# Kernel tuning notes

Measured on AMD Instinct MI355X. Metric: run time of the kernel, lower is better.

## Reference

```python
import jax, jax.numpy as jnp
import numpy as np


def setup_inputs() -> dict:
    key = jax.random.key(0)
    k0, k1, k2 = jax.random.split(key, 3)
    B, N, C, H = 4, 4096, 384, 192  # H = encoder_channel // 2
    point = jax.random.normal(k0, (B, N, 3), dtype=jnp.float32)
    W1 = jax.random.normal(k1, (6, H), dtype=jnp.float32) * (1.0 / np.sqrt(6.0))
    b1 = jnp.zeros((H,), dtype=jnp.float32)
    W2 = jax.random.normal(k2, (H, C), dtype=jnp.float32) * (1.0 / np.sqrt(H))
    b2 = jnp.zeros((C,), dtype=jnp.float32)
    return {"point": point, "W1": W1, "b1": b1, "W2": W2, "b2": b2, "k": 16}


def reference(point, W1, b1, W2, b2, k):
    # point: [B, N, 3]
    # pairwise squared distances [B, N, N]
    diff = point[:, :, None, :] - point[:, None, :, :]
    dist = jnp.sum(diff * diff, axis=-1)
    # torch: distance.argsort()[:, :, :k]  (includes self as nearest)
    idx = jnp.argsort(dist, axis=-1)[:, :, :k]          # [B, N, k]
    # gather neighbor coordinates per batch: [B, N, k, 3]
    neigh = jax.vmap(lambda p, i: p[i])(point, idx)
    rel = neigh - point[:, :, None, :]                   # relative coords
    ctr = jnp.broadcast_to(point[:, :, None, :], rel.shape)
    f = jnp.concatenate([rel, ctr], axis=-1)             # [B, N, k, 6]
    # Mlp: fc1 -> swish -> fc2 (dropout p=0)
    h = f @ W1 + b1
    h = h * jax.nn.sigmoid(h)
    h = h @ W2 + b2                                      # [B, N, k, C]
    return jnp.max(h, axis=-2)                           # [B, N, C]
```

## Files before the change

kernel.cpp:

```cpp
#include <hip/hip_runtime.h>

#define NPTS 4096
#define NBATCH 4
#define HDIM 192
#define CDIM 384

typedef _Float16 f16x8 __attribute__((ext_vector_type(8)));
typedef float f32x4 __attribute__((ext_vector_type(4)));

__global__ __launch_bounds__(256) void prep_w2(const float* __restrict__ W2,
                                               _Float16* __restrict__ W2F) {
  const int j = blockIdx.x * 256 + threadIdx.x;
  if (j < 9216) {
    const int lane = j & 63, r = lane & 15, kg = lane >> 4;
    const int kt = (j >> 6) % 6, ct = j / 384;
    const int c = ct * 16 + r, h0 = kt * 32 + kg * 8;
    f16x8 v;
#pragma unroll
    for (int e = 0; e < 8; ++e) v[e] = (_Float16)W2[(size_t)(h0 + e) * CDIM + c];
    *(f16x8*)(W2F + (size_t)j * 8) = v;
  }
}

#define SCAP 30
#define FINF 3.4e38f

#define PRUNE()                                                                      \
  do {                                                                               \
    int mc = cnt;                                                                    \
    _Pragma("unroll")                                                                \
    for (int s = 32; s; s >>= 1) { int o = __shfl_xor(mc, s); mc = mc > o ? mc : o; }\
    mc = __builtin_amdgcn_readfirstlane(mc);                                         \
    for (int e = 0; e < mc; ++e) {                                                   \
      const int j = sstk[sbase + e] & 4095;                                          \
      const float dx = qx - spx[j];                                                  \
      const float dy = qy - spy[j];                                                  \
      const float dz = qz - spz[j];                                                  \
      const float d = __fadd_rn(__fadd_rn(__fmul_rn(dx, dx), __fmul_rn(dy, dy)),     \
                                __fmul_rn(dz, dz));                                  \
      const float v = (e < cnt && d < dl[15]) ? d : FINF;                            \
      bool cc[16];                                                                   \
      _Pragma("unroll")                                                              \
      for (int i = 0; i < 16; ++i) cc[i] = v < dl[i];                                \
      _Pragma("unroll")                                                              \
      for (int i = 15; i >= 1; --i) {                                                \
        dl[i] = cc[i] ? (cc[i - 1] ? dl[i - 1] : v) : dl[i];                         \
        il[i] = cc[i] ? (cc[i - 1] ? il[i - 1] : j) : il[i];                         \
      }                                                                              \
      dl[0] = cc[0] ? v : dl[0];                                                     \
      il[0] = cc[0] ? j : il[0];                                                     \
    }                                                                                \
    cnt = 0;                                                                         \
    thr = dl[15];                                                                    \
    atomicMin(&sThrU[ql], __float_as_uint(dl[15]));                                  \
  } while (0)

__global__ __launch_bounds__(512) void knn_kernel(const float* __restrict__ pts,
                                                  int* __restrict__ idx_out) {
  __shared__ float smem[12352];
  __shared__ float sstk_f[7680];
  __shared__ unsigned sThrU[32];
  unsigned short* sstk = (unsigned short*)sstk_f;

  float* spx = smem;
  float* spy = smem + 4096;
  float* spz = smem + 8192;

  const int t  = threadIdx.x;
  const int b  = blockIdx.x >> 7;
  const int qb = (blockIdx.x & 127) << 5;
  const float* P = pts + (size_t)b * NPTS * 3;

  for (int i = t; i < NPTS; i += 512) {
    spx[i] = P[3 * i + 0];
    spy[i] = P[3 * i + 1];
    spz[i] = P[3 * i + 2];
  }
  if (t < 32) sThrU[t] = __float_as_uint(FINF);
  __syncthreads();

  const int ql    = t & 31;
  const int q     = qb + ql;
  const int cid   = (t >> 5) & 15;
  const int cbase = cid << 8;
  const float qx = spx[q], qy = spy[q], qz = spz[q];

  float dl[16];
  int   il[16];
#pragma unroll
  for (int i = 0; i < 16; ++i) { dl[i] = FINF; il[i] = 0; }
  float thr = FINF;
  int   cnt = 0;
  const int sbase = t * SCAP;

  for (int jt = 0; jt < 256; jt += 8) {
    {
      const unsigned tb = ((volatile unsigned*)sThrU)[ql];
      thr = fminf(dl[15], __uint_as_float(tb));
    }
    const int jb = cbase + jt;
    const f32x4 x0 = *(const f32x4*)(spx + jb);
    const f32x4 x1 = *(const f32x4*)(spx + jb + 4);
    const f32x4 y0 = *(const f32x4*)(spy + jb);
    const f32x4 y1 = *(const f32x4*)(spy + jb + 4);
    const f32x4 z0 = *(const f32x4*)(spz + jb);
    const f32x4 z1 = *(const f32x4*)(spz + jb + 4);
#pragma unroll
    for (int u = 0; u < 8; ++u) {
      const float px = (u < 4) ? x0[u & 3] : x1[u & 3];
      const float py = (u < 4) ? y0[u & 3] : y1[u & 3];
      const float pz = (u < 4) ? z0[u & 3] : z1[u & 3];
      const float dx = qx - px;
      const float dy = qy - py;
      const float dz = qz - pz;
      const float d = __fadd_rn(__fadd_rn(__fmul_rn(dx, dx), __fmul_rn(dy, dy)),
                                __fmul_rn(dz, dz));
      if (d <= thr) { sstk[sbase + cnt] = (unsigned short)(jb + u); ++cnt; }
    }
    if (__any(cnt >= SCAP - 8)) PRUNE();
  }
  PRUNE();

  __syncthreads();

  float*          md = smem;
  unsigned short* mi = (unsigned short*)(smem + 8224);
  const int lbase = ql * 257 + cid * 16;
#pragma unroll
  for (int i = 0; i < 16; ++i) {
    md[lbase + i] = dl[i];
    mi[lbase + i] = (unsigned short)il[i];
  }
  __syncthreads();

  float*          od = sstk_f;
  unsigned short* oi = (unsigned short*)(sstk_f + 2080);
  if (t < 128) {
    const int mq = t >> 2, g = t & 3;
    const int base = mq * 257 + g * 64;
    int p0 = 0, p1 = 0, p2 = 0, p3 = 0;
    const int ob = mq * 65 + g * 16;
    for (int r = 0; r < 16; ++r) {
      const float d0 = md[base + p0];
      const float d1 = md[base + 16 + p1];
      const float d2 = md[base + 32 + p2];
      const float d3 = md[base + 48 + p3];
      int bw = 0; float bd = d0;
      if (d1 < bd) { bd = d1; bw = 1; }
      if (d2 < bd) { bd = d2; bw = 2; }
      if (d3 < bd) { bd = d3; bw = 3; }
      const unsigned short bi = (bw == 0) ? mi[base + p0]
                              : (bw == 1) ? mi[base + 16 + p1]
                              : (bw == 2) ? mi[base + 32 + p2]
                                          : mi[base + 48 + p3];
      od[ob + r] = bd;
      oi[ob + r] = bi;
      p0 += (bw == 0); p1 += (bw == 1); p2 += (bw == 2); p3 += (bw == 3);
    }
  }
  __syncthreads();

  if (t < 32) {
    const int base = t * 65;
    int p0 = 0, p1 = 0, p2 = 0, p3 = 0;
    int* op = idx_out + (((size_t)b * NPTS + qb + t) << 4);
    for (int r = 0; r < 16; ++r) {
      const float d0 = od[base + p0];
      const float d1 = od[base + 16 + p1];
      const float d2 = od[base + 32 + p2];
      const float d3 = od[base + 48 + p3];
      int bw = 0; float bd = d0;
      if (d1 < bd) { bd = d1; bw = 1; }
      if (d2 < bd) { bd = d2; bw = 2; }
      if (d3 < bd) { bd = d3; bw = 3; }
      const unsigned short bi = (bw == 0) ? oi[base + p0]
                              : (bw == 1) ? oi[base + 16 + p1]
                              : (bw == 2) ? oi[base + 32 + p2]
                                          : oi[base + 48 + p3];
      op[r] = (int)bi;
      p0 += (bw == 0); p1 += (bw == 1); p2 += (bw == 2); p3 += (bw == 3);
    }
  }
}

__global__ __launch_bounds__(512) void mlp_kernel(const float* __restrict__ pts,
                                                  const int* __restrict__ idx,
                                                  const float* __restrict__ W1,
                                                  const float* __restrict__ b1,
                                                  const _Float16* __restrict__ W2F,
                                                  const float* __restrict__ b2,
                                                  float* __restrict__ out) {
  __shared__ _Float16 sB[73728];

  const int bid = blockIdx.x;
  const int b   = bid >> 7;
  const int t   = threadIdx.x;
  const int wv  = t >> 6;
  const int q0  = ((bid & 127) << 5) + (wv << 2);
  const float* P = pts + (size_t)b * NPTS * 3;
  const int l   = t & 63;
  const int r   = l & 15;
  const int kg  = l >> 4;

#pragma unroll
  for (int i = 0; i < 18; ++i) {
    const int j = i * 512 + t;
    *(f16x8*)(sB + (size_t)j * 8) = *(const f16x8*)(W2F + (size_t)j * 8);
  }

  float f[4][6];
#pragma unroll
  for (int qi = 0; qi < 4; ++qi) {
    const int qq = q0 + qi;
    const int nb = idx[(((size_t)b * NPTS + qq) << 4) + r];
    const float ax = P[qq * 3 + 0], ay = P[qq * 3 + 1], az = P[qq * 3 + 2];
    f[qi][0] = P[nb * 3 + 0] - ax;
    f[qi][1] = P[nb * 3 + 1] - ay;
    f[qi][2] = P[nb * 3 + 2] - az;
    f[qi][3] = ax; f[qi][4] = ay; f[qi][5] = az;
  }

  f16x8 af[4][6];
#pragma unroll
  for (int kt = 0; kt < 6; ++kt) {
    const int h0 = kt * 32 + kg * 8;
    const f32x4 bb0 = *(const f32x4*)(b1 + h0);
    const f32x4 bb1 = *(const f32x4*)(b1 + h0 + 4);
    f32x4 w0[6], w1[6];
#pragma unroll
    for (int in = 0; in < 6; ++in) {
      w0[in] = *(const f32x4*)(W1 + in * HDIM + h0);
      w1[in] = *(const f32x4*)(W1 + in * HDIM + h0 + 4);
    }
#pragma unroll
    for (int qi = 0; qi < 4; ++qi) {
      f32x4 a0 = bb0, a1 = bb1;
#pragma unroll
      for (int in = 0; in < 6; ++in) {
        a0 += f[qi][in] * w0[in];
        a1 += f[qi][in] * w1[in];
      }
      f16x8 v;
#pragma unroll
      for (int j = 0; j < 4; ++j) {
        v[j]     = (_Float16)(a0[j] * __builtin_amdgcn_rcpf(1.0f + __expf(-a0[j])));
        v[j + 4] = (_Float16)(a1[j] * __builtin_amdgcn_rcpf(1.0f + __expf(-a1[j])));
      }
      af[qi][kt] = v;
    }
  }
  __syncthreads();

  const size_t orow = (size_t)b * NPTS + q0;
  const _Float16* bp = sB + (size_t)l * 8;

  for (int ct = 0; ct < 24; ++ct) {
    const int c = ct * 16 + r;
    f16x8 bfr[6];
#pragma unroll
    for (int kt = 0; kt < 6; ++kt)
      bfr[kt] = *(const f16x8*)(bp + (size_t)(ct * 6 + kt) * 512);

    f32x4 acc[4];
#pragma unroll
    for (int qi = 0; qi < 4; ++qi) acc[qi] = f32x4{0.f, 0.f, 0.f, 0.f};
#pragma unroll
    for (int kt = 0; kt < 6; ++kt)
#pragma unroll
      for (int qi = 0; qi < 4; ++qi)
        acc[qi] = __builtin_amdgcn_mfma_f32_16x16x32_f16(af[qi][kt], bfr[kt], acc[qi], 0, 0, 0);

    const float bb = b2[c];
#pragma unroll
    for (int qi = 0; qi < 4; ++qi) {
      float m = fmaxf(fmaxf(acc[qi][0], acc[qi][1]), fmaxf(acc[qi][2], acc[qi][3]));
      m = fmaxf(m, __shfl_xor(m, 16));
      m = fmaxf(m, __shfl_xor(m, 32));
      if (l < 16)
        out[(orow + qi) * CDIM + c] = m + bb;
    }
  }
}

extern "C" void kernel_launch(void* const* d_in, const int* in_sizes, int n_in,
                              void* d_out, int out_size, void* d_ws, size_t ws_size,
                              hipStream_t stream) {
  const float* point = (const float*)d_in[0];
  const float* W1    = (const float*)d_in[1];
  const float* b1    = (const float*)d_in[2];
  const float* W2    = (const float*)d_in[3];
  const float* b2    = (const float*)d_in[4];

  int*      idx_ws = (int*)d_ws;
  _Float16* W2F    = (_Float16*)((char*)d_ws + (1 << 20));

  prep_w2<<<36, 256, 0, stream>>>(W2, W2F);
  knn_kernel<<<512, 512, 0, stream>>>(point, idx_ws);
  mlp_kernel<<<512, 512, 0, stream>>>(point, idx_ws, W1, b1, W2F, b2, (float*)d_out);
}
```

Before: 149.0 us.

## Sort points by x and prune kNN search slabs by coordinate gap

```diff
diff --git a/kernel.cpp b/kernel.cpp
--- a/kernel.cpp
+++ b/kernel.cpp
@@ -4,6 +4,7 @@
 #define NBATCH 4
 #define HDIM 192
 #define CDIM 384
+#define FINF 3.4e38f
 
 typedef _Float16 f16x8 __attribute__((ext_vector_type(8)));
 typedef float f32x4 __attribute__((ext_vector_type(4)));
@@ -22,162 +23,207 @@
   }
 }
 
-#define SCAP 30
-#define FINF 3.4e38f
-
-#define PRUNE()                                                                      \
-  do {                                                                               \
-    int mc = cnt;                                                                    \
-    _Pragma("unroll")                                                                \
-    for (int s = 32; s; s >>= 1) { int o = __shfl_xor(mc, s); mc = mc > o ? mc : o; }\
-    mc = __builtin_amdgcn_readfirstlane(mc);                                         \
-    for (int e = 0; e < mc; ++e) {                                                   \
-      const int j = sstk[sbase + e] & 4095;                                          \
-      const float dx = qx - spx[j];                                                  \
-      const float dy = qy - spy[j];                                                  \
-      const float dz = qz - spz[j];                                                  \
-      const float d = __fadd_rn(__fadd_rn(__fmul_rn(dx, dx), __fmul_rn(dy, dy)),     \
-                                __fmul_rn(dz, dz));                                  \
-      const float v = (e < cnt && d < dl[15]) ? d : FINF;                            \
-      bool cc[16];                                                                   \
-      _Pragma("unroll")                                                              \
-      for (int i = 0; i < 16; ++i) cc[i] = v < dl[i];                                \
-      _Pragma("unroll")                                                              \
-      for (int i = 15; i >= 1; --i) {                                                \
-        dl[i] = cc[i] ? (cc[i - 1] ? dl[i - 1] : v) : dl[i];                         \
-        il[i] = cc[i] ? (cc[i - 1] ? il[i - 1] : j) : il[i];                         \
-      }                                                                              \
-      dl[0] = cc[0] ? v : dl[0];                                                     \
-      il[0] = cc[0] ? j : il[0];                                                     \
-    }                                                                                \
-    cnt = 0;                                                                         \
-    thr = dl[15];                                                                    \
-    atomicMin(&sThrU[ql], __float_as_uint(dl[15]));                                  \
+__global__ __launch_bounds__(1024) void sort_kernel(const float* __restrict__ pts,
+                                                    float4* __restrict__ sp4) {
+  __shared__ float kx[4096];
+  __shared__ int   ki[4096];
+  const int b = blockIdx.x;
+  const float* P = pts + (size_t)b * NPTS * 3;
+  const int t = threadIdx.x;
+  for (int i = t; i < 4096; i += 1024) { kx[i] = P[3 * i]; ki[i] = i; }
+  __syncthreads();
+  for (int k = 2; k <= 4096; k <<= 1) {
+    for (int jj = k >> 1; jj > 0; jj >>= 1) {
+      for (int m = t; m < 2048; m += 1024) {
+        const int i = ((m & ~(jj - 1)) << 1) | (m & (jj - 1));
+        const int p = i | jj;
+        const bool up = (i & k) == 0;
+        const float xi = kx[i], xp = kx[p];
+        const int   ii = ki[i], ip = ki[p];
+        const bool gt = (xi > xp) || (xi == xp && ii > ip);
+        if (gt == up) { kx[i] = xp; kx[p] = xi; ki[i] = ip; ki[p] = ii; }
+      }
+      __syncthreads();
+    }
+  }
+  for (int i = t; i < 4096; i += 1024) {
+    const int j = ki[i];
+    sp4[(size_t)b * 4096 + i] =
+        make_float4(P[3 * j], P[3 * j + 1], P[3 * j + 2], __uint_as_float((unsigned)j));
+  }
+}
+
+#define KSCAP 32
+
+#define PRUNE2()                                                                      \
+  do {                                                                                \
+    int mc = cnt;                                                                     \
+    _Pragma("unroll")                                                                 \
+    for (int s_ = 32; s_; s_ >>= 1) { int o_ = __shfl_xor(mc, s_); mc = mc > o_ ? mc : o_; } \
+    mc = __builtin_amdgcn_readfirstlane(mc);                                          \
+    for (int e = 0; e < mc; ++e) {                                                    \
+      const bool act = (e < cnt);                                                     \
+      const float    dd = act ? dstk[e * 512 + t] : FINF;                             \
+      const unsigned jj = act ? (unsigned)jstk[e * 512 + t] : 0xFFFFFFFFu;            \
+      bool cc[16];                                                                    \
+      _Pragma("unroll")                                                               \
+      for (int i = 0; i < 16; ++i)                                                    \
+        cc[i] = (dd < dl[i]) || (dd == dl[i] && jj < il[i]);                          \
+      _Pragma("unroll")                                                               \
+      for (int i = 15; i >= 1; --i) {                                                 \
+        dl[i] = cc[i] ? (cc[i - 1] ? dl[i - 1] : dd) : dl[i];                         \
+        il[i] = cc[i] ? (cc[i - 1] ? il[i - 1] : jj) : il[i];                         \
+      }                                                                               \
+      dl[0] = cc[0] ? dd : dl[0];                                                     \
+      il[0] = cc[0] ? jj : il[0];                                                     \
+    }                                                                                 \
+    cnt = 0;                                                                          \
+    thr = dl[15];                                                                     \
+    atomicMin(&sThrU[l], __float_as_uint(dl[15]));                                    \
   } while (0)
 
-__global__ __launch_bounds__(512) void knn_kernel(const float* __restrict__ pts,
+#define PROC_SLAB(S)                                                                  \
+  do {                                                                                \
+    slab[wv][l] = SP[(S) * 64 + l];               \
+    for (int c0 = 0; c0 < 64; c0 += 16) {                                             \
+      const float te = fminf(thr, __uint_as_float(((volatile unsigned*)sThrU)[l]));   \
+      _Pragma("unroll")                                                               \
+      for (int c = c0; c < c0 + 16; ++c) {                                            \
+        const float4 pc = slab[wv][c];                                                \
+        const float dx = qx - pc.x;                                                   \
+        const float dy = qy - pc.y;                                                   \
+        const float dz = qz - pc.z;                                                   \
+                  \
+        const float d = __fadd_rn(__fadd_rn(__fmul_rn(dx, dx), __fmul_rn(dy, dy)),    \
+                                  __fmul_rn(dz, dz));                                 \
+        if (d <= te) {                                                                \
+          dstk[cnt * 512 + t] = d;                                                    \
+          jstk[cnt * 512 + t] = (unsigned short)__float_as_uint(pc.w);                \
+          ++cnt;                                                                      \
+        }                                                                             \
+      }                                                                               \
+      if (__any(cnt >= KSCAP - 16)) PRUNE2();                                         \
+    }                                                                                 \
+  } while (0)
+
+__global__ __launch_bounds__(512) void knn_kernel(const float4* __restrict__ sp4,
                                                   int* __restrict__ idx_out) {
-  __shared__ float smem[12352];
-  __shared__ float sstk_f[7680];
-  __shared__ unsigned sThrU[32];
-  unsigned short* sstk = (unsigned short*)sstk_f;
-
-  float* spx = smem;
-  float* spy = smem + 4096;
-  float* spz = smem + 8192;
-
-  const int t  = threadIdx.x;
-  const int b  = blockIdx.x >> 7;
-  const int qb = (blockIdx.x & 127) << 5;
-  const float* P = pts + (size_t)b * NPTS * 3;
-
-  for (int i = t; i < NPTS; i += 512) {
-    spx[i] = P[3 * i + 0];
-    spy[i] = P[3 * i + 1];
-    spz[i] = P[3 * i + 2];
-  }
-  if (t < 32) sThrU[t] = __float_as_uint(FINF);
-  __syncthreads();
-
-  const int ql    = t & 31;
-  const int q     = qb + ql;
-  const int cid   = (t >> 5) & 15;
-  const int cbase = cid << 8;
-  const float qx = spx[q], qy = spy[q], qz = spz[q];
-
-  float dl[16];
-  int   il[16];
-#pragma unroll
-  for (int i = 0; i < 16; ++i) { dl[i] = FINF; il[i] = 0; }
+  __shared__ float          dstk[KSCAP * 512];
+  __shared__ unsigned short jstk[KSCAP * 512];
+  __shared__ unsigned       sThrU[64];
+  __shared__ float4         slab[8][64];
+
+  const int bid = blockIdx.x;
+  const int b = bid >> 6, g = bid & 63;
+  const float4* SP = sp4 + (size_t)b * 4096;
+  const int t = threadIdx.x, wv = t >> 6, l = t & 63;
+
+  if (t < 64) sThrU[t] = __float_as_uint(FINF);
+  __syncthreads();
+
+  const float4 me = SP[g * 64 + l];
+  const float qx = me.x, qy = me.y, qz = me.z;
+  const unsigned origq = __float_as_uint(me.w);
+
+  float    dl[16];
+  unsigned il[16];
+#pragma unroll
+  for (int i = 0; i < 16; ++i) { dl[i] = FINF; il[i] = 0xFFFFFFFFu; }
   float thr = FINF;
   int   cnt = 0;
-  const int sbase = t * SCAP;
-
-  for (int jt = 0; jt < 256; jt += 8) {
-    {
-      const unsigned tb = ((volatile unsigned*)sThrU)[ql];
-      thr = fminf(dl[15], __uint_as_float(tb));
-    }
-    const int jb = cbase + jt;
-    const f32x4 x0 = *(const f32x4*)(spx + jb);
-    const f32x4 x1 = *(const f32x4*)(spx + jb + 4);
-    const f32x4 y0 = *(const f32x4*)(spy + jb);
-    const f32x4 y1 = *(const f32x4*)(spy + jb + 4);
-    const f32x4 z0 = *(const f32x4*)(spz + jb);
-    const f32x4 z1 = *(const f32x4*)(spz + jb + 4);
-#pragma unroll
-    for (int u = 0; u < 8; ++u) {
-      const float px = (u < 4) ? x0[u & 3] : x1[u & 3];
-      const float py = (u < 4) ? y0[u & 3] : y1[u & 3];
-      const float pz = (u < 4) ? z0[u & 3] : z1[u & 3];
-      const float dx = qx - px;
-      const float dy = qy - py;
-      const float dz = qz - pz;
-      const float d = __fadd_rn(__fadd_rn(__fmul_rn(dx, dx), __fmul_rn(dy, dy)),
-                                __fmul_rn(dz, dz));
-      if (d <= thr) { sstk[sbase + cnt] = (unsigned short)(jb + u); ++cnt; }
-    }
-    if (__any(cnt >= SCAP - 8)) PRUNE();
-  }
-  PRUNE();
-
-  __syncthreads();
-
-  float*          md = smem;
-  unsigned short* mi = (unsigned short*)(smem + 8224);
-  const int lbase = ql * 257 + cid * 16;
-#pragma unroll
-  for (int i = 0; i < 16; ++i) {
-    md[lbase + i] = dl[i];
-    mi[lbase + i] = (unsigned short)il[i];
-  }
-  __syncthreads();
-
-  float*          od = sstk_f;
-  unsigned short* oi = (unsigned short*)(sstk_f + 2080);
-  if (t < 128) {
-    const int mq = t >> 2, g = t & 3;
-    const int base = mq * 257 + g * 64;
+
+  int  oHi = wv;
+  int  oLo = (wv == 0) ? 8 : wv;
+  bool hiOpen = (g + oHi) < 64;
+  bool loOpen = (g - oLo) >= 0;
+
+  while (hiOpen || loOpen) {
+    if (hiOpen) {
+      const int s = g + oHi;
+      bool skip = false;
+      if (oHi > 0) {
+        const float bx  = SP[s * 64].x;
+        const float gap = bx - qx;
+        const float te  = fminf(thr, __uint_as_float(((volatile unsigned*)sThrU)[l]));
+        skip = __all(__fmul_rn(gap, gap) > te * 1.0001f + 1e-6f);
+      }
+      if (skip) hiOpen = false;
+      else {
+        PROC_SLAB(s);
+        oHi += 8;
+        if (g + oHi >= 64) hiOpen = false;
+      }
+    }
+    if (loOpen) {
+      const int s = g - oLo;
+      {
+        const float bx  = SP[s * 64 + 63].x;
+        const float gap = qx - bx;
+        const float te  = fminf(thr, __uint_as_float(((volatile unsigned*)sThrU)[l]));
+        if (__all(__fmul_rn(gap, gap) > te * 1.0001f + 1e-6f)) loOpen = false;
+      }
+      if (loOpen) {
+        PROC_SLAB(s);
+        oLo += 8;
+        if (g - oLo < 0) loOpen = false;
+      }
+    }
+  }
+  PRUNE2();
+
+  __syncthreads();
+
+  float*          dm = dstk;
+  unsigned short* jm = jstk;
+  {
+    const int base = l * 129 + wv * 16;
+#pragma unroll
+    for (int i = 0; i < 16; ++i) {
+      dm[base + i] = dl[i];
+      jm[base + i] = (unsigned short)il[i];
+    }
+  }
+  __syncthreads();
+
+  float*          om = dstk + 8320;
+  unsigned short* oj = jstk + 8320;
+  if (t < 256) {
+    const int q = t >> 2, h = t & 3;
+    const int bse = q * 129 + h * 32;
+    int p0 = 0, p1 = 0;
+    const int ob = q * 65 + h * 16;
+    for (int r = 0; r < 16; ++r) {
+      const float d0 = dm[bse + p0];
+      const float d1 = dm[bse + 16 + p1];
+      const unsigned short j0 = jm[bse + p0];
+      const unsigned short j1 = jm[bse + 16 + p1];
+      const bool take1 = (d1 < d0) || (d1 == d0 && j1 < j0);
+      om[ob + r] = take1 ? d1 : d0;
+      oj[ob + r] = take1 ? j1 : j0;
+      p0 += !take1; p1 += take1;
+    }
+  }
+  __syncthreads();
+
+  if (t < 64) {
+    const int bse = t * 65;
     int p0 = 0, p1 = 0, p2 = 0, p3 = 0;
-    const int ob = mq * 65 + g * 16;
+    const unsigned oq = __float_as_uint(SP[g * 64 + t].w);
+    int* op = idx_out + (((size_t)b * NPTS + oq) << 4);
     for (int r = 0; r < 16; ++r) {
-      const float d0 = md[base + p0];
-      const float d1 = md[base + 16 + p1];
-      const float d2 = md[base + 32 + p2];
-      const float d3 = md[base + 48 + p3];
-      int bw = 0; float bd = d0;
-      if (d1 < bd) { bd = d1; bw = 1; }
-      if (d2 < bd) { bd = d2; bw = 2; }
-      if (d3 < bd) { bd = d3; bw = 3; }
-      const unsigned short bi = (bw == 0) ? mi[base + p0]
-                              : (bw == 1) ? mi[base + 16 + p1]
-                              : (bw == 2) ? mi[base + 32 + p2]
-                                          : mi[base + 48 + p3];
-      od[ob + r] = bd;
-      oi[ob + r] = bi;
-      p0 += (bw == 0); p1 += (bw == 1); p2 += (bw == 2); p3 += (bw == 3);
-    }
-  }
-  __syncthreads();
-
-  if (t < 32) {
-    const int base = t * 65;
-    int p0 = 0, p1 = 0, p2 = 0, p3 = 0;
-    int* op = idx_out + (((size_t)b * NPTS + qb + t) << 4);
-    for (int r = 0; r < 16; ++r) {
-      const float d0 = od[base + p0];
-      const float d1 = od[base + 16 + p1];
-      const float d2 = od[base + 32 + p2];
-      const float d3 = od[base + 48 + p3];
-      int bw = 0; float bd = d0;
-      if (d1 < bd) { bd = d1; bw = 1; }
-      if (d2 < bd) { bd = d2; bw = 2; }
-      if (d3 < bd) { bd = d3; bw = 3; }
-      const unsigned short bi = (bw == 0) ? oi[base + p0]
-                              : (bw == 1) ? oi[base + 16 + p1]
-                              : (bw == 2) ? oi[base + 32 + p2]
-                                          : oi[base + 48 + p3];
-      op[r] = (int)bi;
+      const float d0 = om[bse + p0];
+      const float d1 = om[bse + 16 + p1];
+      const float d2 = om[bse + 32 + p2];
+      const float d3 = om[bse + 48 + p3];
+      const unsigned short j0 = oj[bse + p0];
+      const unsigned short j1 = oj[bse + 16 + p1];
+      const unsigned short j2 = oj[bse + 32 + p2];
+      const unsigned short j3 = oj[bse + 48 + p3];
+      float bd = d0; unsigned short bj = j0; int bw = 0;
+      if (d1 < bd || (d1 == bd && j1 < bj)) { bd = d1; bj = j1; bw = 1; }
+      if (d2 < bd || (d2 == bd && j2 < bj)) { bd = d2; bj = j2; bw = 2; }
+      if (d3 < bd || (d3 == bd && j3 < bj)) { bd = d3; bj = j3; bw = 3; }
+      op[r] = (int)bj;
       p0 += (bw == 0); p1 += (bw == 1); p2 += (bw == 2); p3 += (bw == 3);
     }
   }
@@ -292,9 +338,11 @@
   const float* b2    = (const float*)d_in[4];
 
   int*      idx_ws = (int*)d_ws;
-  _Float16* W2F    = (_Float16*)((char*)d_ws + (1 << 20));
+  float4*   sp4    = (float4*)((char*)d_ws + (1 << 20));
+  _Float16* W2F    = (_Float16*)((char*)d_ws + (1 << 20) + (256 << 10));
 
   prep_w2<<<36, 256, 0, stream>>>(W2, W2F);
-  knn_kernel<<<512, 512, 0, stream>>>(point, idx_ws);
+  sort_kernel<<<NBATCH, 1024, 0, stream>>>(point, sp4);
+  knn_kernel<<<256, 512, 0, stream>>>(sp4, idx_ws);
   mlp_kernel<<<512, 512, 0, stream>>>(point, idx_ws, W1, b1, W2F, b2, (float*)d_out);
 }
```

Result: slower. 262.2 us (+76.0%).

## Sort points into x-buckets and prune kNN chunks by bounding gap

Applied to the files above, without the earlier changes.

```diff
diff --git a/kernel.cpp b/kernel.cpp
--- a/kernel.cpp
+++ b/kernel.cpp
@@ -4,6 +4,7 @@
 #define NBATCH 4
 #define HDIM 192
 #define CDIM 384
+#define FINF 3.4e38f
 
 typedef _Float16 f16x8 __attribute__((ext_vector_type(8)));
 typedef float f32x4 __attribute__((ext_vector_type(4)));
@@ -22,100 +23,185 @@
   }
 }
 
-#define SCAP 30
-#define FINF 3.4e38f
+__global__ __launch_bounds__(1024) void bucket_kernel(const float* __restrict__ pts,
+                                                      float4* __restrict__ sp4,
+                                                      float* __restrict__ bnds) {
+  __shared__ float sx[4096];
+  __shared__ float sxs[4096];
+  __shared__ unsigned hist[64];
+  __shared__ float rmn_s[16], rmx_s[16];
+  __shared__ float gmin_s, ginvw_s;
+  const int b = blockIdx.x;
+  const float* P = pts + (size_t)b * NPTS * 3;
+  const int t = threadIdx.x;
+
+  float mn = FINF, mx = -FINF;
+  for (int i = t; i < 4096; i += 1024) {
+    const float x = P[3 * i];
+    sx[i] = x;
+    mn = fminf(mn, x);
+    mx = fmaxf(mx, x);
+  }
+#pragma unroll
+  for (int s = 32; s; s >>= 1) {
+    mn = fminf(mn, __shfl_xor(mn, s));
+    mx = fmaxf(mx, __shfl_xor(mx, s));
+  }
+  if ((t & 63) == 0) { rmn_s[t >> 6] = mn; rmx_s[t >> 6] = mx; }
+  if (t < 64) hist[t] = 0;
+  __syncthreads();
+  if (t == 0) {
+    float gmn = rmn_s[0], gmx = rmx_s[0];
+    for (int i = 1; i < 16; ++i) { gmn = fminf(gmn, rmn_s[i]); gmx = fmaxf(gmx, rmx_s[i]); }
+    gmin_s  = gmn;
+    ginvw_s = (gmx > gmn) ? 64.0f / (gmx - gmn) : 0.0f;
+  }
+  __syncthreads();
+  const float gmn = gmin_s, ginvw = ginvw_s;
+  for (int i = t; i < 4096; i += 1024) {
+    int bn = (int)((sx[i] - gmn) * ginvw);
+    bn = bn < 0 ? 0 : (bn > 63 ? 63 : bn);
+    atomicAdd(&hist[bn], 1u);
+  }
+  __syncthreads();
+  if (t == 0) {
+    unsigned run = 0;
+    for (int i = 0; i < 64; ++i) { const unsigned c = hist[i]; hist[i] = run; run += c; }
+  }
+  __syncthreads();
+  for (int i = t; i < 4096; i += 1024) {
+    const float x = sx[i];
+    int bn = (int)((x - gmn) * ginvw);
+    bn = bn < 0 ? 0 : (bn > 63 ? 63 : bn);
+    const unsigned pos = atomicAdd(&hist[bn], 1u);
+    sp4[(size_t)b * 4096 + pos] =
+        make_float4(x, P[3 * i + 1], P[3 * i + 2], __uint_as_float((unsigned)i));
+    sxs[pos] = x;
+  }
+  __syncthreads();
+  {
+    const int rg = t >> 6, ln = t & 63;
+    float rmn = FINF, rmx = -FINF;
+    for (int k = ln; k < 256; k += 64) {
+      const float v = sxs[rg * 256 + k];
+      rmn = fminf(rmn, v);
+      rmx = fmaxf(rmx, v);
+    }
+#pragma unroll
+    for (int s = 32; s; s >>= 1) {
+      rmn = fminf(rmn, __shfl_xor(rmn, s));
+      rmx = fmaxf(rmx, __shfl_xor(rmx, s));
+    }
+    if (ln == 0) { bnds[b * 32 + rg * 2] = rmn; bnds[b * 32 + rg * 2 + 1] = rmx; }
+  }
+}
+
+#define SCAP 15
 
 #define PRUNE()                                                                      \
   do {                                                                               \
     int mc = cnt;                                                                    \
     _Pragma("unroll")                                                                \
-    for (int s = 32; s; s >>= 1) { int o = __shfl_xor(mc, s); mc = mc > o ? mc : o; }\
+    for (int s_ = 32; s_; s_ >>= 1) { int o_ = __shfl_xor(mc, s_); mc = mc > o_ ? mc : o_; } \
     mc = __builtin_amdgcn_readfirstlane(mc);                                         \
     for (int e = 0; e < mc; ++e) {                                                   \
-      const int j = sstk[sbase + e] & 4095;                                          \
-      const float dx = qx - spx[j];                                                  \
-      const float dy = qy - spy[j];                                                  \
-      const float dz = qz - spz[j];                                                  \
+      const int s = sstk[sbase + e] & 4095;                                          \
+      const float dx = qx - spx[s];                                                  \
+      const float dy = qy - spy[s];                                                  \
+      const float dz = qz - spz[s];                                                  \
       const float d = __fadd_rn(__fadd_rn(__fmul_rn(dx, dx), __fmul_rn(dy, dy)),     \
                                 __fmul_rn(dz, dz));                                  \
-      const float v = (e < cnt && d < dl[15]) ? d : FINF;                            \
+      const bool act = (e < cnt);                                                    \
+      const float    dd = act ? d : FINF;                                            \
+      const unsigned jj = act ? spw[s] : 0xFFFFFFFFu;                                \
       bool cc[16];                                                                   \
       _Pragma("unroll")                                                              \
-      for (int i = 0; i < 16; ++i) cc[i] = v < dl[i];                                \
+      for (int i = 0; i < 16; ++i)                                                   \
+        cc[i] = (dd < dl[i]) || (dd == dl[i] && jj < il[i]);                         \
       _Pragma("unroll")                                                              \
       for (int i = 15; i >= 1; --i) {                                                \
-        dl[i] = cc[i] ? (cc[i - 1] ? dl[i - 1] : v) : dl[i];                         \
-        il[i] = cc[i] ? (cc[i - 1] ? il[i - 1] : j) : il[i];                         \
+        dl[i] = cc[i] ? (cc[i - 1] ? dl[i - 1] : dd) : dl[i];                        \
+        il[i] = cc[i] ? (cc[i - 1] ? il[i - 1] : jj) : il[i];                        \
       }                                                                              \
-      dl[0] = cc[0] ? v : dl[0];                                                     \
-      il[0] = cc[0] ? j : il[0];                                                     \
+      dl[0] = cc[0] ? dd : dl[0];                                                    \
+      il[0] = cc[0] ? jj : il[0];                                                    \
     }                                                                                \
     cnt = 0;                                                                         \
     thr = dl[15];                                                                    \
-    atomicMin(&sThrU[ql], __float_as_uint(dl[15]));                                  \
+    atomicMin(&sThrU[ql], __float_as_uint(thr));                                     \
   } while (0)
 
-__global__ __launch_bounds__(512) void knn_kernel(const float* __restrict__ pts,
+__global__ __launch_bounds__(512) void knn_kernel(const float4* __restrict__ sp4,
+                                                  const float* __restrict__ bnds,
                                                   int* __restrict__ idx_out) {
-  __shared__ float smem[12352];
-  __shared__ float sstk_f[7680];
+  __shared__ float smem[16384];
+  __shared__ unsigned short sstk[7680];
   __shared__ unsigned sThrU[32];
-  unsigned short* sstk = (unsigned short*)sstk_f;
-
-  float* spx = smem;
-  float* spy = smem + 4096;
-  float* spz = smem + 8192;
+
+  float*    spx = smem;
+  float*    spy = smem + 4096;
+  float*    spz = smem + 8192;
+  unsigned* spw = (unsigned*)(smem + 12288);
 
   const int t  = threadIdx.x;
   const int b  = blockIdx.x >> 7;
-  const int qb = (blockIdx.x & 127) << 5;
-  const float* P = pts + (size_t)b * NPTS * 3;
-
-  for (int i = t; i < NPTS; i += 512) {
-    spx[i] = P[3 * i + 0];
-    spy[i] = P[3 * i + 1];
-    spz[i] = P[3 * i + 2];
+  const int g  = blockIdx.x & 127;
+  const float4* SP = sp4 + (size_t)b * 4096;
+
+  for (int i = t; i < 4096; i += 512) {
+    const float4 v = SP[i];
+    spx[i] = v.x; spy[i] = v.y; spz[i] = v.z;
+    spw[i] = __float_as_uint(v.w);
   }
   if (t < 32) sThrU[t] = __float_as_uint(FINF);
   __syncthreads();
 
   const int ql    = t & 31;
-  const int q     = qb + ql;
   const int cid   = (t >> 5) & 15;
   const int cbase = cid << 8;
-  const float qx = spx[q], qy = spy[q], qz = spz[q];
-
-  float dl[16];
-  int   il[16];
-#pragma unroll
-  for (int i = 0; i < 16; ++i) { dl[i] = FINF; il[i] = 0; }
+  const int qpos  = g * 32 + ql;
+  const float qx = spx[qpos], qy = spy[qpos], qz = spz[qpos];
+  const unsigned oq = spw[qpos];
+
+  const float cmin = bnds[b * 32 + cid * 2];
+  const float cmax = bnds[b * 32 + cid * 2 + 1];
+  const float gapc = fmaxf(fmaxf(cmin - qx, qx - cmax), 0.0f);
+  const float g2   = __fmul_rn(gapc, gapc);
+
+  float    dl[16];
+  unsigned il[16];
+#pragma unroll
+  for (int i = 0; i < 16; ++i) { dl[i] = FINF; il[i] = 0xFFFFFFFFu; }
   float thr = FINF;
   int   cnt = 0;
   const int sbase = t * SCAP;
+  bool fin = false;
 
   for (int jt = 0; jt < 256; jt += 8) {
-    {
-      const unsigned tb = ((volatile unsigned*)sThrU)[ql];
-      thr = fminf(dl[15], __uint_as_float(tb));
-    }
-    const int jb = cbase + jt;
-    const f32x4 x0 = *(const f32x4*)(spx + jb);
-    const f32x4 x1 = *(const f32x4*)(spx + jb + 4);
-    const f32x4 y0 = *(const f32x4*)(spy + jb);
-    const f32x4 y1 = *(const f32x4*)(spy + jb + 4);
-    const f32x4 z0 = *(const f32x4*)(spz + jb);
-    const f32x4 z1 = *(const f32x4*)(spz + jb + 4);
-#pragma unroll
-    for (int u = 0; u < 8; ++u) {
-      const float px = (u < 4) ? x0[u & 3] : x1[u & 3];
-      const float py = (u < 4) ? y0[u & 3] : y1[u & 3];
-      const float pz = (u < 4) ? z0[u & 3] : z1[u & 3];
-      const float dx = qx - px;
-      const float dy = qy - py;
-      const float dz = qz - pz;
-      const float d = __fadd_rn(__fadd_rn(__fmul_rn(dx, dx), __fmul_rn(dy, dy)),
-                                __fmul_rn(dz, dz));
-      if (d <= thr) { sstk[sbase + cnt] = (unsigned short)(jb + u); ++cnt; }
+    const unsigned tb = ((volatile unsigned*)sThrU)[ql];
+    const float te = fminf(thr, __uint_as_float(tb));
+    fin = fin || (g2 > te * 1.0001f + 1e-6f);
+    if (__all(fin)) break;
+    if (!fin) {
+      const int jb = cbase + jt;
+      const f32x4 x0 = *(const f32x4*)(spx + jb);
+      const f32x4 x1 = *(const f32x4*)(spx + jb + 4);
+      const f32x4 y0 = *(const f32x4*)(spy + jb);
+      const f32x4 y1 = *(const f32x4*)(spy + jb + 4);
+      const f32x4 z0 = *(const f32x4*)(spz + jb);
+      const f32x4 z1 = *(const f32x4*)(spz + jb + 4);
+#pragma unroll
+      for (int u = 0; u < 8; ++u) {
+        const float px = (u < 4) ? x0[u & 3] : x1[u & 3];
+        const float py = (u < 4) ? y0[u & 3] : y1[u & 3];
+        const float pz = (u < 4) ? z0[u & 3] : z1[u & 3];
+        const float dx = qx - px;
+        const float dy = qy - py;
+        const float dz = qz - pz;
+        const float d = __fadd_rn(__fadd_rn(__fmul_rn(dx, dx), __fmul_rn(dy, dy)),
+                                  __fmul_rn(dz, dz));
+        if (d <= te) { sstk[sbase + cnt] = (unsigned short)(jb + u); ++cnt; }
+      }
     }
     if (__any(cnt >= SCAP - 8)) PRUNE();
   }
@@ -125,36 +211,38 @@
 
   float*          md = smem;
   unsigned short* mi = (unsigned short*)(smem + 8224);
-  const int lbase = ql * 257 + cid * 16;
-#pragma unroll
-  for (int i = 0; i < 16; ++i) {
-    md[lbase + i] = dl[i];
-    mi[lbase + i] = (unsigned short)il[i];
-  }
-  __syncthreads();
-
-  float*          od = sstk_f;
-  unsigned short* oi = (unsigned short*)(sstk_f + 2080);
+  {
+    const int lbase = ql * 257 + cid * 16;
+#pragma unroll
+    for (int i = 0; i < 16; ++i) {
+      md[lbase + i] = dl[i];
+      mi[lbase + i] = (unsigned short)il[i];
+    }
+  }
+  __syncthreads();
+
+  float*          od = (float*)sstk;
+  unsigned short* oj = (unsigned short*)((char*)sstk + 8320);
   if (t < 128) {
-    const int mq = t >> 2, g = t & 3;
-    const int base = mq * 257 + g * 64;
+    const int mq = t >> 2, grp = t & 3;
+    const int base = mq * 257 + grp * 64;
     int p0 = 0, p1 = 0, p2 = 0, p3 = 0;
-    const int ob = mq * 65 + g * 16;
+    const int ob = mq * 65 + grp * 16;
     for (int r = 0; r < 16; ++r) {
       const float d0 = md[base + p0];
       const float d1 = md[base + 16 + p1];
       const float d2 = md[base + 32 + p2];
       const float d3 = md[base + 48 + p3];
-      int bw = 0; float bd = d0;
-      if (d1 < bd) { bd = d1; bw = 1; }
-      if (d2 < bd) { bd = d2; bw = 2; }
-      if (d3 < bd) { bd = d3; bw = 3; }
-      const unsigned short bi = (bw == 0) ? mi[base + p0]
-                              : (bw == 1) ? mi[base + 16 + p1]
-                              : (bw == 2) ? mi[base + 32 + p2]
-                                          : mi[base + 48 + p3];
+      const unsigned short j0 = mi[base + p0];
+      const unsigned short j1 = mi[base + 16 + p1];
+      const unsigned short j2 = mi[base + 32 + p2];
+      const unsigned short j3 = mi[base + 48 + p3];
+      float bd = d0; unsigned short bj = j0; int bw = 0;
+      if (d1 < bd || (d1 == bd && j1 < bj)) { bd = d1; bj = j1; bw = 1; }
+      if (d2 < bd || (d2 == bd && j2 < bj)) { bd = d2; bj = j2; bw = 2; }
+      if (d3 < bd || (d3 == bd && j3 < bj)) { bd = d3; bj = j3; bw = 3; }
       od[ob + r] = bd;
-      oi[ob + r] = bi;
+      oj[ob + r] = bj;
       p0 += (bw == 0); p1 += (bw == 1); p2 += (bw == 2); p3 += (bw == 3);
     }
   }
@@ -163,21 +251,21 @@
   if (t < 32) {
     const int base = t * 65;
     int p0 = 0, p1 = 0, p2 = 0, p3 = 0;
-    int* op = idx_out + (((size_t)b * NPTS + qb + t) << 4);
+    int* op = idx_out + (((size_t)b * NPTS + oq) << 4);
     for (int r = 0; r < 16; ++r) {
       const float d0 = od[base + p0];
       const float d1 = od[base + 16 + p1];
       const float d2 = od[base + 32 + p2];
       const float d3 = od[base + 48 + p3];
-      int bw = 0; float bd = d0;
-      if (d1 < bd) { bd = d1; bw = 1; }
-      if (d2 < bd) { bd = d2; bw = 2; }
-      if (d3 < bd) { bd = d3; bw = 3; }
-      const unsigned short bi = (bw == 0) ? oi[base + p0]
-                              : (bw == 1) ? oi[base + 16 + p1]
-                              : (bw == 2) ? oi[base + 32 + p2]
-                                          : oi[base + 48 + p3];
-      op[r] = (int)bi;
+      const unsigned short j0 = oj[base + p0];
+      const unsigned short j1 = oj[base + 16 + p1];
+      const unsigned short j2 = oj[base + 32 + p2];
+      const unsigned short j3 = oj[base + 48 + p3];
+      float bd = d0; unsigned short bj = j0; int bw = 0;
+      if (d1 < bd || (d1 == bd && j1 < bj)) { bd = d1; bj = j1; bw = 1; }
+      if (d2 < bd || (d2 == bd && j2 < bj)) { bd = d2; bj = j2; bw = 2; }
+      if (d3 < bd || (d3 == bd && j3 < bj)) { bd = d3; bj = j3; bw = 3; }
+      op[r] = (int)bj;
       p0 += (bw == 0); p1 += (bw == 1); p2 += (bw == 2); p3 += (bw == 3);
     }
   }
@@ -292,9 +380,12 @@
   const float* b2    = (const float*)d_in[4];
 
   int*      idx_ws = (int*)d_ws;
-  _Float16* W2F    = (_Float16*)((char*)d_ws + (1 << 20));
+  float4*   sp4    = (float4*)((char*)d_ws + (1 << 20));
+  _Float16* W2F    = (_Float16*)((char*)d_ws + (1 << 20) + (256 << 10));
+  float*    bnds   = (float*)((char*)d_ws + (1 << 20) + (512 << 10));
 
   prep_w2<<<36, 256, 0, stream>>>(W2, W2F);
-  knn_kernel<<<512, 512, 0, stream>>>(point, idx_ws);
+  bucket_kernel<<<NBATCH, 1024, 0, stream>>>(point, sp4, bnds);
+  knn_kernel<<<512, 512, 0, stream>>>(sp4, bnds, idx_ws);
   mlp_kernel<<<512, 512, 0, stream>>>(point, idx_ws, W1, b1, W2F, b2, (float*)d_out);
 }
```

Measured after the change: 264.9 us. 77.8% more time.

## Use 1024-thread MLP blocks with two query rounds to amortize W2 staging

Applied to the files above, without the earlier changes.

```diff
diff --git a/kernel.cpp b/kernel.cpp
--- a/kernel.cpp
+++ b/kernel.cpp
@@ -183,101 +183,99 @@
   }
 }
 
-__global__ __launch_bounds__(512) void mlp_kernel(const float* __restrict__ pts,
-                                                  const int* __restrict__ idx,
-                                                  const float* __restrict__ W1,
-                                                  const float* __restrict__ b1,
-                                                  const _Float16* __restrict__ W2F,
-                                                  const float* __restrict__ b2,
-                                                  float* __restrict__ out) {
+__global__ __launch_bounds__(1024) void mlp_kernel(const float* __restrict__ pts,
+                                                   const int* __restrict__ idx,
+                                                   const float* __restrict__ W1,
+                                                   const float* __restrict__ b1,
+                                                   const _Float16* __restrict__ W2F,
+                                                   const float* __restrict__ b2,
+                                                   float* __restrict__ out) {
   __shared__ _Float16 sB[73728];
 
   const int bid = blockIdx.x;
-  const int b   = bid >> 7;
+  const int b   = bid >> 6;
   const int t   = threadIdx.x;
   const int wv  = t >> 6;
-  const int q0  = ((bid & 127) << 5) + (wv << 2);
-  const float* P = pts + (size_t)b * NPTS * 3;
   const int l   = t & 63;
   const int r   = l & 15;
   const int kg  = l >> 4;
-
-#pragma unroll
-  for (int i = 0; i < 18; ++i) {
-    const int j = i * 512 + t;
+  const float* P = pts + (size_t)b * NPTS * 3;
+
+#pragma unroll
+  for (int i = 0; i < 9; ++i) {
+    const int j = i * 1024 + t;
     *(f16x8*)(sB + (size_t)j * 8) = *(const f16x8*)(W2F + (size_t)j * 8);
   }
 
-  float f[4][6];
-#pragma unroll
-  for (int qi = 0; qi < 4; ++qi) {
-    const int qq = q0 + qi;
-    const int nb = idx[(((size_t)b * NPTS + qq) << 4) + r];
-    const float ax = P[qq * 3 + 0], ay = P[qq * 3 + 1], az = P[qq * 3 + 2];
-    f[qi][0] = P[nb * 3 + 0] - ax;
-    f[qi][1] = P[nb * 3 + 1] - ay;
-    f[qi][2] = P[nb * 3 + 2] - az;
-    f[qi][3] = ax; f[qi][4] = ay; f[qi][5] = az;
-  }
-
-  f16x8 af[4][6];
-#pragma unroll
-  for (int kt = 0; kt < 6; ++kt) {
-    const int h0 = kt * 32 + kg * 8;
-    const f32x4 bb0 = *(const f32x4*)(b1 + h0);
-    const f32x4 bb1 = *(const f32x4*)(b1 + h0 + 4);
-    f32x4 w0[6], w1[6];
-#pragma unroll
-    for (int in = 0; in < 6; ++in) {
-      w0[in] = *(const f32x4*)(W1 + in * HDIM + h0);
-      w1[in] = *(const f32x4*)(W1 + in * HDIM + h0 + 4);
-    }
-#pragma unroll
-    for (int qi = 0; qi < 4; ++qi) {
-      f32x4 a0 = bb0, a1 = bb1;
-#pragma unroll
-      for (int in = 0; in < 6; ++in) {
-        a0 += f[qi][in] * w0[in];
-        a1 += f[qi][in] * w1[in];
+  const _Float16* bp = sB + (size_t)l * 8;
+
+  for (int rnd = 0; rnd < 2; ++rnd) {
+    const int q0 = ((bid & 63) << 6) + (rnd << 5) + (wv << 1);
+
+    float f[2][6];
+#pragma unroll
+    for (int qi = 0; qi < 2; ++qi) {
+      const int qq = q0 + qi;
+      const int nb = idx[(((size_t)b * NPTS + qq) << 4) + r];
+      const float ax = P[qq * 3 + 0], ay = P[qq * 3 + 1], az = P[qq * 3 + 2];
+      f[qi][0] = P[nb * 3 + 0] - ax;
+      f[qi][1] = P[nb * 3 + 1] - ay;
+      f[qi][2] = P[nb * 3 + 2] - az;
+      f[qi][3] = ax; f[qi][4] = ay; f[qi][5] = az;
+    }
+
+    f16x8 af[2][6];
+#pragma unroll
+    for (int kt = 0; kt < 6; ++kt) {
+      const int h0 = kt * 32 + kg * 8;
+#pragma unroll
+      for (int qi = 0; qi < 2; ++qi) {
+        f32x4 a0 = *(const f32x4*)(b1 + h0);
+        f32x4 a1 = *(const f32x4*)(b1 + h0 + 4);
+#pragma unroll
+        for (int in = 0; in < 6; ++in) {
+          a0 += f[qi][in] * *(const f32x4*)(W1 + in * HDIM + h0);
+          a1 += f[qi][in] * *(const f32x4*)(W1 + in * HDIM + h0 + 4);
+        }
+        f16x8 v;
+#pragma unroll
+        for (int j = 0; j < 4; ++j) {
+          v[j]     = (_Float16)(a0[j] * __builtin_amdgcn_rcpf(1.0f + __expf(-a0[j])));
+          v[j + 4] = (_Float16)(a1[j] * __builtin_amdgcn_rcpf(1.0f + __expf(-a1[j])));
+        }
+        af[qi][kt] = v;
       }
-      f16x8 v;
-#pragma unroll
-      for (int j = 0; j < 4; ++j) {
-        v[j]     = (_Float16)(a0[j] * __builtin_amdgcn_rcpf(1.0f + __expf(-a0[j])));
-        v[j + 4] = (_Float16)(a1[j] * __builtin_amdgcn_rcpf(1.0f + __expf(-a1[j])));
+    }
+
+    if (rnd == 0) __syncthreads();
+
+    const size_t orow = (size_t)b * NPTS + q0;
+    for (int ct = 0; ct < 24; ++ct) {
+      const int c = ct * 16 + r;
+      f16x8 bfr[6];
+#pragma unroll
+      for (int kt = 0; kt < 6; ++kt)
+        bfr[kt] = *(const f16x8*)(bp + (size_t)(ct * 6 + kt) * 512);
+
+      f32x4 acc0 = {0.f, 0.f, 0.f, 0.f};
+      f32x4 acc1 = {0.f, 0.f, 0.f, 0.f};
+#pragma unroll
+      for (int kt = 0; kt < 6; ++kt) {
+        acc0 = __builtin_amdgcn_mfma_f32_16x16x32_f16(af[0][kt], bfr[kt], acc0, 0, 0, 0);
+        acc1 = __builtin_amdgcn_mfma_f32_16x16x32_f16(af[1][kt], bfr[kt], acc1, 0, 0, 0);
       }
-      af[qi][kt] = v;
-    }
-  }
-  __syncthreads();
-
-  const size_t orow = (size_t)b * NPTS + q0;
-  const _Float16* bp = sB + (size_t)l * 8;
-
-  for (int ct = 0; ct < 24; ++ct) {
-    const int c = ct * 16 + r;
-    f16x8 bfr[6];
-#pragma unroll
-    for (int kt = 0; kt < 6; ++kt)
-      bfr[kt] = *(const f16x8*)(bp + (size_t)(ct * 6 + kt) * 512);
-
-    f32x4 acc[4];
-#pragma unroll
-    for (int qi = 0; qi < 4; ++qi) acc[qi] = f32x4{0.f, 0.f, 0.f, 0.f};
-#pragma unroll
-    for (int kt = 0; kt < 6; ++kt)
-#pragma unroll
-      for (int qi = 0; qi < 4; ++qi)
-        acc[qi] = __builtin_amdgcn_mfma_f32_16x16x32_f16(af[qi][kt], bfr[kt], acc[qi], 0, 0, 0);
-
-    const float bb = b2[c];
-#pragma unroll
-    for (int qi = 0; qi < 4; ++qi) {
-      float m = fmaxf(fmaxf(acc[qi][0], acc[qi][1]), fmaxf(acc[qi][2], acc[qi][3]));
-      m = fmaxf(m, __shfl_xor(m, 16));
-      m = fmaxf(m, __shfl_xor(m, 32));
-      if (l < 16)
-        out[(orow + qi) * CDIM + c] = m + bb;
+
+      const float bb = b2[c];
+      float m0 = fmaxf(fmaxf(acc0[0], acc0[1]), fmaxf(acc0[2], acc0[3]));
+      m0 = fmaxf(m0, __shfl_xor(m0, 16));
+      m0 = fmaxf(m0, __shfl_xor(m0, 32));
+      float m1 = fmaxf(fmaxf(acc1[0], acc1[1]), fmaxf(acc1[2], acc1[3]));
+      m1 = fmaxf(m1, __shfl_xor(m1, 16));
+      m1 = fmaxf(m1, __shfl_xor(m1, 32));
+      if (l < 16) {
+        out[(orow + 0) * CDIM + c] = m0 + bb;
+        out[(orow + 1) * CDIM + c] = m1 + bb;
+      }
     }
   }
 }
@@ -296,5 +294,5 @@
 
   prep_w2<<<36, 256, 0, stream>>>(W2, W2F);
   knn_kernel<<<512, 512, 0, stream>>>(point, idx_ws);
-  mlp_kernel<<<512, 512, 0, stream>>>(point, idx_ws, W1, b1, W2F, b2, (float*)d_out);
-}
+  mlp_kernel<<<256, 1024, 0, stream>>>(point, idx_ws, W1, b1, W2F, b2, (float*)d_out);
+}
```

New measurement: 502.4 us. 3.37x slower.
